# Kernel tuning notes

Measured on AMD Instinct MI355X. Metric: run time of the kernel, lower is better.

Reference implementation:

```python
import jax, jax.numpy as jnp
import numpy as np

N_NODES = 50000


def setup_inputs() -> dict:
    key = jax.random.key(0)
    k1, k2, k3, k4, k5 = jax.random.split(key, 5)
    d_in, d_out, n_edges = 128, 128, 800000
    x = jax.random.normal(k1, (N_NODES, d_in), dtype=jnp.float32)
    edge_index = jax.random.randint(k2, (2, n_edges), 0, N_NODES, dtype=jnp.int64)
    # Glorot-ish init for linear weights, bias zeros-like small normal
    W_l = jax.random.normal(k3, (d_in, d_out), dtype=jnp.float32) / np.sqrt(d_in)
    W_r = jax.random.normal(k4, (d_in, d_out), dtype=jnp.float32) / np.sqrt(d_in)
    b = jax.random.normal(k5, (d_out,), dtype=jnp.float32) * 0.01
    return {"x": x, "edge_index": edge_index, "W_l": W_l, "W_r": W_r, "b": b}


def reference(x, edge_index, W_l, W_r, b):
    # PyG SAGEConv (aggr='mean', root_weight=True, bias=True):
    #   out_i = W_l @ mean_{j: (j->i) in E} x_j + b + W_r @ x_i
    # followed by ReLU (GConv act) and dropout(p=0.0, eval) == identity.
    src, dst = edge_index[0], edge_index[1]
    msgs = x[src]                                            # [E, d_in] gather
    agg_sum = jax.ops.segment_sum(msgs, dst, num_segments=N_NODES)  # [N, d_in]
    deg = jax.ops.segment_sum(jnp.ones_like(dst, dtype=x.dtype), dst,
                              num_segments=N_NODES)          # [N]
    agg_mean = agg_sum / jnp.maximum(deg, 1.0)[:, None]      # zero for isolated nodes
    z = agg_mean @ W_l + b + x @ W_r                         # [N, d_out]
    return jax.nn.relu(z)
```

## Files before the change

kernel.cpp:

```cpp
#include <hip/hip_runtime.h>

#define N_NODES 50000
#define D 128
#define NC 128
#define SCANB 196

typedef short bf16x8 __attribute__((ext_vector_type(8)));
typedef float f32x4 __attribute__((ext_vector_type(4)));
typedef float f32x2 __attribute__((ext_vector_type(2)));

__device__ __forceinline__ ushort f2bf(float f) {
    uint u = __float_as_uint(f);
    u += 0x7FFF + ((u >> 16) & 1);
    return (ushort)(u >> 16);
}

__device__ __forceinline__ void addrow_fp8(int4 q, float* a) {
    f32x2 p;
    p = __builtin_amdgcn_cvt_pk_f32_fp8(q.x, false); a[0]  += p.x; a[1]  += p.y;
    p = __builtin_amdgcn_cvt_pk_f32_fp8(q.x, true);  a[2]  += p.x; a[3]  += p.y;
    p = __builtin_amdgcn_cvt_pk_f32_fp8(q.y, false); a[4]  += p.x; a[5]  += p.y;
    p = __builtin_amdgcn_cvt_pk_f32_fp8(q.y, true);  a[6]  += p.x; a[7]  += p.y;
    p = __builtin_amdgcn_cvt_pk_f32_fp8(q.z, false); a[8]  += p.x; a[9]  += p.y;
    p = __builtin_amdgcn_cvt_pk_f32_fp8(q.z, true);  a[10] += p.x; a[11] += p.y;
    p = __builtin_amdgcn_cvt_pk_f32_fp8(q.w, false); a[12] += p.x; a[13] += p.y;
    p = __builtin_amdgcn_cvt_pk_f32_fp8(q.w, true);  a[14] += p.x; a[15] += p.y;
}

__global__ __launch_bounds__(256) void convert_kernel(const float* __restrict__ x,
                                                      const float* __restrict__ Wl,
                                                      const float* __restrict__ Wr,
                                                      ushort* __restrict__ x_bf,
                                                      int* __restrict__ x_fp8,
                                                      ushort* __restrict__ Btf) {
    const int i = blockIdx.x * 256 + threadIdx.x;
    if (i < (N_NODES * D) / 4) {
        float4 v = ((const float4*)x)[i];
        ushort4 o;
        o.x = f2bf(v.x); o.y = f2bf(v.y); o.z = f2bf(v.z); o.w = f2bf(v.w);
        ((ushort4*)x_bf)[i] = o;
        int p = __builtin_amdgcn_cvt_pk_fp8_f32(v.x, v.y, 0, false);
        p = __builtin_amdgcn_cvt_pk_fp8_f32(v.z, v.w, p, true);
        x_fp8[i] = p;
    }
    if (i < 32768) {
        int j  = i & 7;
        int l  = (i >> 3) & 63;
        int nf = (i >> 9) & 7;
        int ks = (i >> 12) & 7;
        int lr = l & 15, kb = l >> 4;
        int col  = nf * 16 + lr;
        int kloc = (ks & 3) * 32 + kb * 8 + j;
        const float* W = (ks < 4) ? Wl : Wr;
        Btf[i] = f2bf(W[kloc * D + col]);
    }
}

__global__ __launch_bounds__(256) void countA_kernel(const int* __restrict__ dst,
                                                     ushort* __restrict__ partial,
                                                     int E, int chunk) {
    __shared__ uint cnt[N_NODES / 2];
    const int t = threadIdx.x;
    const int b = blockIdx.x;
    for (int k = t; k < N_NODES / 2; k += 256) cnt[k] = 0;
    __syncthreads();
    const int e0 = b * chunk;
    const int e1 = min(E, e0 + chunk);
    for (int e = e0 + t; e < e1; e += 256) {
        int d = dst[e];
        atomicAdd(&cnt[d >> 1], 1u << ((d & 1) << 4));
    }
    __syncthreads();
    uint* pu = (uint*)(partial + (size_t)b * N_NODES);
    for (int k = t; k < N_NODES / 2; k += 256) pu[k] = cnt[k];
}

__global__ __launch_bounds__(256) void scanAB_kernel(const ushort* __restrict__ partial,
                                                     ushort* __restrict__ cumbase,
                                                     int* __restrict__ offsets,
                                                     int* __restrict__ blocksums) {
    __shared__ int wsums[4];
    __shared__ int wbase[4];
    const int t = threadIdx.x;
    const int lane = t & 63;
    const int wid = t >> 6;
    const int n = blockIdx.x * 256 + t;

    int s = 0;
    if (n < N_NODES) {
        #pragma unroll 4
        for (int c = 0; c < NC; ++c) {
            int v = (int)partial[(size_t)c * N_NODES + n];
            cumbase[(size_t)c * N_NODES + n] = (ushort)s;
            s += v;
        }
    }
    int sc = s;
    #pragma unroll
    for (int off = 1; off < 64; off <<= 1) {
        int u = __shfl_up(sc, off);
        if (lane >= off) sc += u;
    }
    if (lane == 63) wsums[wid] = sc;
    __syncthreads();
    if (t == 0) {
        int c = 0;
        #pragma unroll
        for (int w = 0; w < 4; ++w) { int tmp = wsums[w]; wbase[w] = c; c += tmp; }
        blocksums[blockIdx.x] = c;
    }
    __syncthreads();
    if (n < N_NODES) offsets[n] = wbase[wid] + sc - s;
}

__global__ __launch_bounds__(256) void scanBC2_kernel(int* __restrict__ offsets,
                                                      const int* __restrict__ blocksums,
                                                      int E) {
    __shared__ int ws2[4];
    __shared__ int sbase;
    const int t = threadIdx.x;
    const int lane = t & 63;
    const int wid = t >> 6;
    const int b = blockIdx.x;
    int v = (t < b) ? blocksums[t] : 0;
    #pragma unroll
    for (int off = 32; off > 0; off >>= 1) v += __shfl_down(v, off);
    if (lane == 0) ws2[wid] = v;
    __syncthreads();
    if (t == 0) sbase = ws2[0] + ws2[1] + ws2[2] + ws2[3];
    __syncthreads();
    const int n = b * 256 + t;
    if (n < N_NODES) offsets[n] += sbase;
    if (b == SCANB - 1 && t == 0) offsets[N_NODES] = E;
}

__global__ __launch_bounds__(256) void scatterC_kernel(const int* __restrict__ src,
                                                       const int* __restrict__ dst,
                                                       const int* __restrict__ offsets,
                                                       const ushort* __restrict__ cumbase,
                                                       ushort* __restrict__ sorted_src,
                                                       int E, int chunk) {
    __shared__ uint cnt[N_NODES / 2];
    const int t = threadIdx.x;
    const int b = blockIdx.x;
    for (int k = t; k < N_NODES / 2; k += 256) cnt[k] = 0;
    __syncthreads();
    const ushort* cb = cumbase + (size_t)b * N_NODES;
    const int e0 = b * chunk;
    const int e1 = min(E, e0 + chunk);
    for (int e = e0 + t; e < e1; e += 256) {
        int d = dst[e];
        uint prev = atomicAdd(&cnt[d >> 1], 1u << ((d & 1) << 4));
        int lrank = (int)((prev >> ((d & 1) << 4)) & 0xFFFFu);
        int pos = offsets[d] + (int)cb[d] + lrank;
        sorted_src[pos] = (ushort)src[e];
    }
}

__global__ __launch_bounds__(256) void aggregate_fp8(const int* __restrict__ x_fp8,
                                                     const ushort* __restrict__ sorted_src,
                                                     const int* __restrict__ offsets,
                                                     ushort* __restrict__ agg_bf) {
    const int g = threadIdx.x >> 3;
    const int j = threadIdx.x & 7;
    const int node = blockIdx.x * 32 + g;
    if (node >= N_NODES) return;
    const int s = offsets[node];
    const int e = offsets[node + 1];

    float a[16];
    #pragma unroll
    for (int k = 0; k < 16; ++k) a[k] = 0.0f;

    const int4* xq = (const int4*)x_fp8;
    int p = s;
    for (; p + 4 <= e; p += 4) {
        int s0 = sorted_src[p + 0];
        int s1 = sorted_src[p + 1];
        int s2 = sorted_src[p + 2];
        int s3 = sorted_src[p + 3];
        int4 q0 = xq[s0 * 8 + j];
        int4 q1 = xq[s1 * 8 + j];
        int4 q2 = xq[s2 * 8 + j];
        int4 q3 = xq[s3 * 8 + j];
        addrow_fp8(q0, a); addrow_fp8(q1, a); addrow_fp8(q2, a); addrow_fp8(q3, a);
    }
    for (; p < e; ++p) {
        int s0 = sorted_src[p];
        int4 q0 = xq[s0 * 8 + j];
        addrow_fp8(q0, a);
    }
    const int dcnt = e - s;
    const float scale = (dcnt > 0) ? (1.0f / (float)dcnt) : 0.0f;
    ushort tmp[16];
    #pragma unroll
    for (int k = 0; k < 16; ++k) tmp[k] = f2bf(a[k] * scale);
    *(int4*)&agg_bf[node * D + j * 16] = ((int4*)tmp)[0];
    *(int4*)&agg_bf[node * D + j * 16 + 8] = ((int4*)tmp)[1];
}

__global__ __launch_bounds__(256) void gemm_direct(const ushort* __restrict__ agg_bf,
                                                   const ushort* __restrict__ x_bf,
                                                   const ushort* __restrict__ Btf,
                                                   const float* __restrict__ bias,
                                                   float* __restrict__ out) {
    const int t = threadIdx.x;
    const int w = t >> 6;
    const int l = t & 63;
    const int lr = l & 15;
    const int kb = l >> 4;
    const int n0 = blockIdx.x * 64;

    int r = n0 + w * 16 + lr;
    if (r >= N_NODES) r = N_NODES - 1;

    f32x4 acc[8] = {};

    #pragma unroll
    for (int ks = 0; ks < 8; ++ks) {
        bf16x8 af = (ks < 4)
            ? *(const bf16x8*)&agg_bf[r * D + ks * 32 + kb * 8]
            : *(const bf16x8*)&x_bf[r * D + (ks - 4) * 32 + kb * 8];
        const ushort* bp = Btf + (size_t)(ks * 8 * 64 + l) * 8;
        #pragma unroll
        for (int nf = 0; nf < 8; ++nf) {
            bf16x8 bfr = *(const bf16x8*)&bp[nf * 64 * 8];
            acc[nf] = __builtin_amdgcn_mfma_f32_16x16x32_bf16(af, bfr, acc[nf], 0, 0, 0);
        }
    }

    #pragma unroll
    for (int nf = 0; nf < 8; ++nf) {
        const int col = nf * 16 + lr;
        const float bb = bias[col];
        #pragma unroll
        for (int i = 0; i < 4; ++i) {
            int row = n0 + w * 16 + kb * 4 + i;
            if (row < N_NODES)
                out[row * D + col] = fmaxf(acc[nf][i] + bb, 0.0f);
        }
    }
}

extern "C" void kernel_launch(void* const* d_in, const int* in_sizes, int n_in,
                              void* d_out, int out_size, void* d_ws, size_t ws_size,
                              hipStream_t stream) {
    const float* x  = (const float*)d_in[0];
    const int*   ei = (const int*)d_in[1];
    const float* Wl = (const float*)d_in[2];
    const float* Wr = (const float*)d_in[3];
    const float* b  = (const float*)d_in[4];
    float* out = (float*)d_out;

    const int E = in_sizes[1] / 2;
    const int* src = ei;
    const int* dst = ei + E;
    const int chunk = (E + NC - 1) / NC;

    char* wsp = (char*)d_ws;
    int*    offsets   = (int*)(wsp + 0);
    int*    blocksums = (int*)(wsp + 200192);
    ushort* sorted    = (ushort*)(wsp + 201216);
    ushort* partial   = (ushort*)(wsp + 1801280);
    ushort* cumbase   = (ushort*)(wsp + 14601280);
    ushort* x_bf      = (ushort*)(wsp + 27401280);
    ushort* agg_bf    = (ushort*)(wsp + 40201280);
    int*    x_fp8     = (int*)(wsp + 53001280);
    ushort* Btf       = (ushort*)(wsp + 59401280);

    convert_kernel<<<(N_NODES * D / 4 + 255) / 256, 256, 0, stream>>>(
        x, Wl, Wr, x_bf, x_fp8, Btf);
    countA_kernel<<<NC, 256, 0, stream>>>(dst, partial, E, chunk);
    scanAB_kernel<<<SCANB, 256, 0, stream>>>(partial, cumbase, offsets, blocksums);
    scanBC2_kernel<<<SCANB, 256, 0, stream>>>(offsets, blocksums, E);
    scatterC_kernel<<<NC, 256, 0, stream>>>(src, dst, offsets, cumbase, sorted, E, chunk);
    aggregate_fp8<<<(N_NODES + 31) / 32, 256, 0, stream>>>(x_fp8, sorted, offsets, agg_bf);
    gemm_direct<<<(N_NODES + 63) / 64, 256, 0, stream>>>(agg_bf, x_bf, Btf, b, out);
}
```

Baseline: 110.6 us.

## Fuse aggregation into GEMM via LDS and fold block-scan base into consumers

Merges the mean-aggregation kernel with the MFMA GEMM, so each block aggregates 64 nodes into a padded LDS tile and feeds it straight to the matrix cores. This removes the bf16 agg buffer round-trip through global memory. The separate block-sum scan kernel is dropped, and each consumer block recomputes the prefix of the block sums serially in shared memory. The count and scatter kernels move to 512 threads. Each thread in the fused kernel now handles 32 features instead of 16, which lowers parallelism in the gather and raises register pressure.

```diff
diff --git a/kernel.cpp b/kernel.cpp
--- a/kernel.cpp
+++ b/kernel.cpp
@@ -56,23 +56,23 @@
     }
 }
 
-__global__ __launch_bounds__(256) void countA_kernel(const int* __restrict__ dst,
+__global__ __launch_bounds__(512) void countA_kernel(const int* __restrict__ dst,
                                                      ushort* __restrict__ partial,
                                                      int E, int chunk) {
     __shared__ uint cnt[N_NODES / 2];
     const int t = threadIdx.x;
     const int b = blockIdx.x;
-    for (int k = t; k < N_NODES / 2; k += 256) cnt[k] = 0;
+    for (int k = t; k < N_NODES / 2; k += 512) cnt[k] = 0;
     __syncthreads();
     const int e0 = b * chunk;
     const int e1 = min(E, e0 + chunk);
-    for (int e = e0 + t; e < e1; e += 256) {
+    for (int e = e0 + t; e < e1; e += 512) {
         int d = dst[e];
         atomicAdd(&cnt[d >> 1], 1u << ((d & 1) << 4));
     }
     __syncthreads();
     uint* pu = (uint*)(partial + (size_t)b * N_NODES);
-    for (int k = t; k < N_NODES / 2; k += 256) pu[k] = cnt[k];
+    for (int k = t; k < N_NODES / 2; k += 512) pu[k] = cnt[k];
 }
 
 __global__ __launch_bounds__(256) void scanAB_kernel(const ushort* __restrict__ partial,
@@ -113,113 +113,117 @@
     if (n < N_NODES) offsets[n] = wbase[wid] + sc - s;
 }
 
-__global__ __launch_bounds__(256) void scanBC2_kernel(int* __restrict__ offsets,
-                                                      const int* __restrict__ blocksums,
-                                                      int E) {
-    __shared__ int ws2[4];
-    __shared__ int sbase;
-    const int t = threadIdx.x;
-    const int lane = t & 63;
-    const int wid = t >> 6;
-    const int b = blockIdx.x;
-    int v = (t < b) ? blocksums[t] : 0;
-    #pragma unroll
-    for (int off = 32; off > 0; off >>= 1) v += __shfl_down(v, off);
-    if (lane == 0) ws2[wid] = v;
-    __syncthreads();
-    if (t == 0) sbase = ws2[0] + ws2[1] + ws2[2] + ws2[3];
-    __syncthreads();
-    const int n = b * 256 + t;
-    if (n < N_NODES) offsets[n] += sbase;
-    if (b == SCANB - 1 && t == 0) offsets[N_NODES] = E;
-}
-
-__global__ __launch_bounds__(256) void scatterC_kernel(const int* __restrict__ src,
+__global__ __launch_bounds__(512) void scatterC_kernel(const int* __restrict__ src,
                                                        const int* __restrict__ dst,
                                                        const int* __restrict__ offsets,
+                                                       const int* __restrict__ blocksums,
                                                        const ushort* __restrict__ cumbase,
                                                        ushort* __restrict__ sorted_src,
                                                        int E, int chunk) {
     __shared__ uint cnt[N_NODES / 2];
+    __shared__ int base[SCANB];
     const int t = threadIdx.x;
     const int b = blockIdx.x;
-    for (int k = t; k < N_NODES / 2; k += 256) cnt[k] = 0;
+    for (int k = t; k < N_NODES / 2; k += 512) cnt[k] = 0;
+    if (t < SCANB) base[t] = blocksums[t];
+    __syncthreads();
+    if (t == 0) {
+        int run = 0;
+        for (int k = 0; k < SCANB; ++k) { int v = base[k]; base[k] = run; run += v; }
+    }
     __syncthreads();
     const ushort* cb = cumbase + (size_t)b * N_NODES;
     const int e0 = b * chunk;
     const int e1 = min(E, e0 + chunk);
-    for (int e = e0 + t; e < e1; e += 256) {
+    for (int e = e0 + t; e < e1; e += 512) {
         int d = dst[e];
         uint prev = atomicAdd(&cnt[d >> 1], 1u << ((d & 1) << 4));
         int lrank = (int)((prev >> ((d & 1) << 4)) & 0xFFFFu);
-        int pos = offsets[d] + (int)cb[d] + lrank;
+        int pos = offsets[d] + base[d >> 8] + (int)cb[d] + lrank;
         sorted_src[pos] = (ushort)src[e];
     }
 }
 
-__global__ __launch_bounds__(256) void aggregate_fp8(const int* __restrict__ x_fp8,
-                                                     const ushort* __restrict__ sorted_src,
-                                                     const int* __restrict__ offsets,
-                                                     ushort* __restrict__ agg_bf) {
-    const int g = threadIdx.x >> 3;
-    const int j = threadIdx.x & 7;
-    const int node = blockIdx.x * 32 + g;
-    if (node >= N_NODES) return;
-    const int s = offsets[node];
-    const int e = offsets[node + 1];
-
-    float a[16];
-    #pragma unroll
-    for (int k = 0; k < 16; ++k) a[k] = 0.0f;
-
-    const int4* xq = (const int4*)x_fp8;
-    int p = s;
-    for (; p + 4 <= e; p += 4) {
-        int s0 = sorted_src[p + 0];
-        int s1 = sorted_src[p + 1];
-        int s2 = sorted_src[p + 2];
-        int s3 = sorted_src[p + 3];
-        int4 q0 = xq[s0 * 8 + j];
-        int4 q1 = xq[s1 * 8 + j];
-        int4 q2 = xq[s2 * 8 + j];
-        int4 q3 = xq[s3 * 8 + j];
-        addrow_fp8(q0, a); addrow_fp8(q1, a); addrow_fp8(q2, a); addrow_fp8(q3, a);
-    }
-    for (; p < e; ++p) {
-        int s0 = sorted_src[p];
-        int4 q0 = xq[s0 * 8 + j];
-        addrow_fp8(q0, a);
-    }
-    const int dcnt = e - s;
-    const float scale = (dcnt > 0) ? (1.0f / (float)dcnt) : 0.0f;
-    ushort tmp[16];
-    #pragma unroll
-    for (int k = 0; k < 16; ++k) tmp[k] = f2bf(a[k] * scale);
-    *(int4*)&agg_bf[node * D + j * 16] = ((int4*)tmp)[0];
-    *(int4*)&agg_bf[node * D + j * 16 + 8] = ((int4*)tmp)[1];
-}
-
-__global__ __launch_bounds__(256) void gemm_direct(const ushort* __restrict__ agg_bf,
-                                                   const ushort* __restrict__ x_bf,
-                                                   const ushort* __restrict__ Btf,
-                                                   const float* __restrict__ bias,
-                                                   float* __restrict__ out) {
-    const int t = threadIdx.x;
+__global__ __launch_bounds__(256) void aggemm2_kernel(const int* __restrict__ x_fp8,
+                                                      const ushort* __restrict__ x_bf,
+                                                      const ushort* __restrict__ sorted_src,
+                                                      const int* __restrict__ offsets,
+                                                      const int* __restrict__ blocksums,
+                                                      const ushort* __restrict__ Btf,
+                                                      const float* __restrict__ bias,
+                                                      float* __restrict__ out, int E) {
+    __shared__ ushort aggT[64][136];
+    __shared__ int base[SCANB];
+    const int t = threadIdx.x;
+    const int n0 = blockIdx.x * 64;
+
+    if (t < SCANB) base[t] = blocksums[t];
+    __syncthreads();
+    if (t == 0) {
+        int run = 0;
+        for (int k = 0; k < SCANB; ++k) { int v = base[k]; base[k] = run; run += v; }
+    }
+    __syncthreads();
+
+    {
+        const int g = t >> 2;
+        const int j = t & 3;
+        const int node = n0 + g;
+        float a[32];
+        #pragma unroll
+        for (int k = 0; k < 32; ++k) a[k] = 0.0f;
+
+        if (node < N_NODES) {
+            const int s = offsets[node] + base[node >> 8];
+            const int np = node + 1;
+            const int e = (np < N_NODES) ? (offsets[np] + base[np >> 8]) : E;
+            const int4* xq = (const int4*)x_fp8;
+            int p = s;
+            for (; p + 4 <= e; p += 4) {
+                int s0 = sorted_src[p + 0];
+                int s1 = sorted_src[p + 1];
+                int s2 = sorted_src[p + 2];
+                int s3 = sorted_src[p + 3];
+                int4 qa0 = xq[s0 * 8 + 2 * j], qb0 = xq[s0 * 8 + 2 * j + 1];
+                int4 qa1 = xq[s1 * 8 + 2 * j], qb1 = xq[s1 * 8 + 2 * j + 1];
+                int4 qa2 = xq[s2 * 8 + 2 * j], qb2 = xq[s2 * 8 + 2 * j + 1];
+                int4 qa3 = xq[s3 * 8 + 2 * j], qb3 = xq[s3 * 8 + 2 * j + 1];
+                addrow_fp8(qa0, a); addrow_fp8(qb0, a + 16);
+                addrow_fp8(qa1, a); addrow_fp8(qb1, a + 16);
+                addrow_fp8(qa2, a); addrow_fp8(qb2, a + 16);
+                addrow_fp8(qa3, a); addrow_fp8(qb3, a + 16);
+            }
+            for (; p < e; ++p) {
+                int s0 = sorted_src[p];
+                int4 qa = xq[s0 * 8 + 2 * j], qb = xq[s0 * 8 + 2 * j + 1];
+                addrow_fp8(qa, a); addrow_fp8(qb, a + 16);
+            }
+            const int dcnt = e - s;
+            const float scale = (dcnt > 0) ? (1.0f / (float)dcnt) : 0.0f;
+            #pragma unroll
+            for (int k = 0; k < 32; ++k) a[k] *= scale;
+        }
+        ushort tmp[32];
+        #pragma unroll
+        for (int k = 0; k < 32; ++k) tmp[k] = f2bf(a[k]);
+        #pragma unroll
+        for (int q = 0; q < 4; ++q)
+            *(int4*)&aggT[g][j * 32 + q * 8] = ((int4*)tmp)[q];
+    }
+    __syncthreads();
+
     const int w = t >> 6;
     const int l = t & 63;
     const int lr = l & 15;
     const int kb = l >> 4;
-    const int n0 = blockIdx.x * 64;
-
-    int r = n0 + w * 16 + lr;
-    if (r >= N_NODES) r = N_NODES - 1;
+    const int rloc = w * 16 + lr;
+    int r = n0 + rloc; if (r >= N_NODES) r = N_NODES - 1;
 
     f32x4 acc[8] = {};
-
     #pragma unroll
     for (int ks = 0; ks < 8; ++ks) {
         bf16x8 af = (ks < 4)
-            ? *(const bf16x8*)&agg_bf[r * D + ks * 32 + kb * 8]
+            ? *(bf16x8*)&aggT[rloc][ks * 32 + kb * 8]
             : *(const bf16x8*)&x_bf[r * D + (ks - 4) * 32 + kb * 8];
         const ushort* bp = Btf + (size_t)(ks * 8 * 64 + l) * 8;
         #pragma unroll
@@ -259,21 +263,20 @@
 
     char* wsp = (char*)d_ws;
     int*    offsets   = (int*)(wsp + 0);
-    int*    blocksums = (int*)(wsp + 200192);
-    ushort* sorted    = (ushort*)(wsp + 201216);
-    ushort* partial   = (ushort*)(wsp + 1801280);
-    ushort* cumbase   = (ushort*)(wsp + 14601280);
-    ushort* x_bf      = (ushort*)(wsp + 27401280);
-    ushort* agg_bf    = (ushort*)(wsp + 40201280);
-    int*    x_fp8     = (int*)(wsp + 53001280);
-    ushort* Btf       = (ushort*)(wsp + 59401280);
+    int*    blocksums = (int*)(wsp + 200704);
+    ushort* sorted    = (ushort*)(wsp + 201728);
+    ushort* partial   = (ushort*)(wsp + 1801760);
+    ushort* cumbase   = (ushort*)(wsp + 14601760);
+    ushort* x_bf      = (ushort*)(wsp + 27401760);
+    int*    x_fp8     = (int*)(wsp + 40201760);
+    ushort* Btf       = (ushort*)(wsp + 46601760);
 
     convert_kernel<<<(N_NODES * D / 4 + 255) / 256, 256, 0, stream>>>(
         x, Wl, Wr, x_bf, x_fp8, Btf);
-    countA_kernel<<<NC, 256, 0, stream>>>(dst, partial, E, chunk);
+    countA_kernel<<<NC, 512, 0, stream>>>(dst, partial, E, chunk);
     scanAB_kernel<<<SCANB, 256, 0, stream>>>(partial, cumbase, offsets, blocksums);
-    scanBC2_kernel<<<SCANB, 256, 0, stream>>>(offsets, blocksums, E);
-    scatterC_kernel<<<NC, 256, 0, stream>>>(src, dst, offsets, cumbase, sorted, E, chunk);
-    aggregate_fp8<<<(N_NODES + 31) / 32, 256, 0, stream>>>(x_fp8, sorted, offsets, agg_bf);
-    gemm_direct<<<(N_NODES + 63) / 64, 256, 0, stream>>>(agg_bf, x_bf, Btf, b, out);
-}
+    scatterC_kernel<<<NC, 512, 0, stream>>>(src, dst, offsets, blocksums, cumbase,
+                                            sorted, E, chunk);
+    aggemm2_kernel<<<(N_NODES + 63) / 64, 256, 0, stream>>>(
+        x_fp8, x_bf, sorted, offsets, blocksums, Btf, b, out, E);
+}
```

Measured after the change: 114.6 us. 1.04x slower.

## Split aggregation across edges and column halves; halve counting-sort chunks

Applied to the files above, without the earlier changes.

The aggregation kernel now gives each node 32 lanes: 8 edge-parallel groups of 4 lanes, with the feature columns split into two halves handled by separate blocks. Partial sums are combined with cross-lane shuffles. This exposes more memory-level parallelism per node for the irregular gathers, at the cost of shuffle reductions and redundant loads of offsets and source indices. The counting-sort phase uses 64 chunks of 512 threads instead of 128 of 256, which shrinks the partial and cumbase arrays the scan must read but gives fewer blocks for the atomics.

```diff
diff --git a/kernel.cpp b/kernel.cpp
--- a/kernel.cpp
+++ b/kernel.cpp
@@ -2,8 +2,9 @@
 
 #define N_NODES 50000
 #define D 128
-#define NC 128
+#define NC 64
 #define SCANB 196
+#define AGG_HALF_BLOCKS 6250
 
 typedef short bf16x8 __attribute__((ext_vector_type(8)));
 typedef float f32x4 __attribute__((ext_vector_type(4)));
@@ -56,23 +57,23 @@
     }
 }
 
-__global__ __launch_bounds__(256) void countA_kernel(const int* __restrict__ dst,
+__global__ __launch_bounds__(512) void countA_kernel(const int* __restrict__ dst,
                                                      ushort* __restrict__ partial,
                                                      int E, int chunk) {
     __shared__ uint cnt[N_NODES / 2];
     const int t = threadIdx.x;
     const int b = blockIdx.x;
-    for (int k = t; k < N_NODES / 2; k += 256) cnt[k] = 0;
+    for (int k = t; k < N_NODES / 2; k += 512) cnt[k] = 0;
     __syncthreads();
     const int e0 = b * chunk;
     const int e1 = min(E, e0 + chunk);
-    for (int e = e0 + t; e < e1; e += 256) {
+    for (int e = e0 + t; e < e1; e += 512) {
         int d = dst[e];
         atomicAdd(&cnt[d >> 1], 1u << ((d & 1) << 4));
     }
     __syncthreads();
     uint* pu = (uint*)(partial + (size_t)b * N_NODES);
-    for (int k = t; k < N_NODES / 2; k += 256) pu[k] = cnt[k];
+    for (int k = t; k < N_NODES / 2; k += 512) pu[k] = cnt[k];
 }
 
 __global__ __launch_bounds__(256) void scanAB_kernel(const ushort* __restrict__ partial,
@@ -134,7 +135,7 @@
     if (b == SCANB - 1 && t == 0) offsets[N_NODES] = E;
 }
 
-__global__ __launch_bounds__(256) void scatterC_kernel(const int* __restrict__ src,
+__global__ __launch_bounds__(512) void scatterC_kernel(const int* __restrict__ src,
                                                        const int* __restrict__ dst,
                                                        const int* __restrict__ offsets,
                                                        const ushort* __restrict__ cumbase,
@@ -143,12 +144,12 @@
     __shared__ uint cnt[N_NODES / 2];
     const int t = threadIdx.x;
     const int b = blockIdx.x;
-    for (int k = t; k < N_NODES / 2; k += 256) cnt[k] = 0;
+    for (int k = t; k < N_NODES / 2; k += 512) cnt[k] = 0;
     __syncthreads();
     const ushort* cb = cumbase + (size_t)b * N_NODES;
     const int e0 = b * chunk;
     const int e1 = min(E, e0 + chunk);
-    for (int e = e0 + t; e < e1; e += 256) {
+    for (int e = e0 + t; e < e1; e += 512) {
         int d = dst[e];
         uint prev = atomicAdd(&cnt[d >> 1], 1u << ((d & 1) << 4));
         int lrank = (int)((prev >> ((d & 1) << 4)) & 0xFFFFu);
@@ -161,42 +162,53 @@
                                                      const ushort* __restrict__ sorted_src,
                                                      const int* __restrict__ offsets,
                                                      ushort* __restrict__ agg_bf) {
-    const int g = threadIdx.x >> 3;
-    const int j = threadIdx.x & 7;
-    const int node = blockIdx.x * 32 + g;
-    if (node >= N_NODES) return;
+    const int b = blockIdx.x;
+    const int half = (b >= AGG_HALF_BLOCKS) ? 1 : 0;
+    const int nb = b - half * AGG_HALF_BLOCKS;
+    const int t = threadIdx.x;
+    const int g = t >> 5;
+    const int l = t & 31;
+    const int j = l & 3;
+    const int ep = l >> 2;
+    const int node = nb * 8 + g;
     const int s = offsets[node];
     const int e = offsets[node + 1];
 
+    const int4* xq = (const int4*)x_fp8;
+    const int coff = half * 4 + j;
+
     float a[16];
     #pragma unroll
     for (int k = 0; k < 16; ++k) a[k] = 0.0f;
 
-    const int4* xq = (const int4*)x_fp8;
-    int p = s;
-    for (; p + 4 <= e; p += 4) {
-        int s0 = sorted_src[p + 0];
-        int s1 = sorted_src[p + 1];
-        int s2 = sorted_src[p + 2];
-        int s3 = sorted_src[p + 3];
-        int4 q0 = xq[s0 * 8 + j];
-        int4 q1 = xq[s1 * 8 + j];
-        int4 q2 = xq[s2 * 8 + j];
-        int4 q3 = xq[s3 * 8 + j];
-        addrow_fp8(q0, a); addrow_fp8(q1, a); addrow_fp8(q2, a); addrow_fp8(q3, a);
-    }
-    for (; p < e; ++p) {
+    int p = s + ep;
+    for (; p + 8 < e; p += 16) {
         int s0 = sorted_src[p];
-        int4 q0 = xq[s0 * 8 + j];
+        int s1 = sorted_src[p + 8];
+        int4 q0 = xq[s0 * 8 + coff];
+        int4 q1 = xq[s1 * 8 + coff];
+        addrow_fp8(q0, a); addrow_fp8(q1, a);
+    }
+    if (p < e) {
+        int s0 = sorted_src[p];
+        int4 q0 = xq[s0 * 8 + coff];
         addrow_fp8(q0, a);
     }
+
+    #pragma unroll
+    for (int k = 0; k < 16; ++k) {
+        a[k] += __shfl_xor(a[k], 4, 32);
+        a[k] += __shfl_xor(a[k], 8, 32);
+        a[k] += __shfl_xor(a[k], 16, 32);
+    }
+
     const int dcnt = e - s;
     const float scale = (dcnt > 0) ? (1.0f / (float)dcnt) : 0.0f;
     ushort tmp[16];
     #pragma unroll
     for (int k = 0; k < 16; ++k) tmp[k] = f2bf(a[k] * scale);
-    *(int4*)&agg_bf[node * D + j * 16] = ((int4*)tmp)[0];
-    *(int4*)&agg_bf[node * D + j * 16 + 8] = ((int4*)tmp)[1];
+    if (ep < 2)
+        *(int4*)&agg_bf[node * D + half * 64 + j * 16 + ep * 8] = ((int4*)tmp)[ep];
 }
 
 __global__ __launch_bounds__(256) void gemm_direct(const ushort* __restrict__ agg_bf,
@@ -259,21 +271,21 @@
 
     char* wsp = (char*)d_ws;
     int*    offsets   = (int*)(wsp + 0);
-    int*    blocksums = (int*)(wsp + 200192);
-    ushort* sorted    = (ushort*)(wsp + 201216);
-    ushort* partial   = (ushort*)(wsp + 1801280);
-    ushort* cumbase   = (ushort*)(wsp + 14601280);
-    ushort* x_bf      = (ushort*)(wsp + 27401280);
-    ushort* agg_bf    = (ushort*)(wsp + 40201280);
-    int*    x_fp8     = (int*)(wsp + 53001280);
-    ushort* Btf       = (ushort*)(wsp + 59401280);
+    int*    blocksums = (int*)(wsp + 200704);
+    ushort* sorted    = (ushort*)(wsp + 201728);
+    ushort* partial   = (ushort*)(wsp + 1801760);
+    ushort* cumbase   = (ushort*)(wsp + 8201760);
+    ushort* x_bf      = (ushort*)(wsp + 14601760);
+    int*    x_fp8     = (int*)(wsp + 27401760);
+    ushort* agg_bf    = (ushort*)(wsp + 33801760);
+    ushort* Btf       = (ushort*)(wsp + 46601760);
 
     convert_kernel<<<(N_NODES * D / 4 + 255) / 256, 256, 0, stream>>>(
         x, Wl, Wr, x_bf, x_fp8, Btf);
-    countA_kernel<<<NC, 256, 0, stream>>>(dst, partial, E, chunk);
+    countA_kernel<<<NC, 512, 0, stream>>>(dst, partial, E, chunk);
     scanAB_kernel<<<SCANB, 256, 0, stream>>>(partial, cumbase, offsets, blocksums);
     scanBC2_kernel<<<SCANB, 256, 0, stream>>>(offsets, blocksums, E);
-    scatterC_kernel<<<NC, 256, 0, stream>>>(src, dst, offsets, cumbase, sorted, E, chunk);
-    aggregate_fp8<<<(N_NODES + 31) / 32, 256, 0, stream>>>(x_fp8, sorted, offsets, agg_bf);
+    scatterC_kernel<<<NC, 512, 0, stream>>>(src, dst, offsets, cumbase, sorted, E, chunk);
+    aggregate_fp8<<<2 * AGG_HALF_BLOCKS, 256, 0, stream>>>(x_fp8, sorted, offsets, agg_bf);
     gemm_direct<<<(N_NODES + 63) / 64, 256, 0, stream>>>(agg_bf, x_bf, Btf, b, out);
 }
```

Result: slower. 140.9 us (+27.4%).
